# Optimization experiments

Measured on AMD Instinct MI355X. Metric: run time of the kernel, lower is better.

## Reference

```python
import jax, jax.numpy as jnp
import numpy as np

EPS = 1e-5

def layer_norm(x, g, b):
    m = jnp.mean(x, axis=-1, keepdims=True)
    v = jnp.var(x, axis=-1, keepdims=True)
    return (x - m) * jax.lax.rsqrt(v + EPS) * g + b

def setup_inputs() -> dict:
    key = jax.random.key(0)
    ks = jax.random.split(key, 10)
    A, T, c_s, c_z, c_atom, c_pair = 1024, 256, 384, 128, 128, 16
    tok = jax.random.randint(ks[0], (A,), 0, T)
    a2t = jax.nn.one_hot(tok, T, dtype=jnp.float32)  # [A, T] one-hot atom->token map
    return {
        "atom_to_token_index": a2t,
        "cl": jax.random.normal(ks[1], (A, c_atom), jnp.float32),
        "plm": jax.random.normal(ks[2], (A, A, c_pair), jnp.float32),
        "ql": jax.random.normal(ks[3], (A, c_atom), jnp.float32),
        "s_trunk": jax.random.normal(ks[4], (T, c_s), jnp.float32),
        "zij": jax.random.normal(ks[5], (T, T, c_z), jnp.float32),
        "rl": jax.random.normal(ks[6], (A, 3), jnp.float32),
        "ln_s_g": jnp.ones((c_s,), jnp.float32),
        "ln_s_b": jnp.zeros((c_s,), jnp.float32),
        "W_s": jax.random.normal(ks[7], (c_s, c_atom), jnp.float32) / np.sqrt(c_s),
        "ln_z_g": jnp.ones((c_z,), jnp.float32),
        "ln_z_b": jnp.zeros((c_z,), jnp.float32),
        "W_z": jax.random.normal(ks[8], (c_z, c_pair), jnp.float32) / np.sqrt(c_z),
        "W_r": jax.random.normal(ks[9], (3, c_atom), jnp.float32) / np.sqrt(3.0),
    }

def reference(atom_to_token_index, cl, plm, ql, s_trunk, zij, rl,
              ln_s_g, ln_s_b, W_s, ln_z_g, ln_z_b, W_z, W_r):
    a2t = atom_to_token_index  # [A, T]
    # token -> atom gather of single rep: sum_t a2t[a,t] * s_trunk[t,:]  -> [A, c_s]
    s_atom = jnp.einsum('at,tc->ac', a2t, s_trunk)
    cl = cl + layer_norm(s_atom, ln_s_g, ln_s_b) @ W_s  # [A, c_atom]
    # token-pair -> atom-pair gather: sum_{t,u} a2t[a,t] a2t[b,u] zij[t,u,:]
    # factored into two one-hot contractions (same math as the dense one-hot outer product)
    z_half = jnp.einsum('at,tuz->auz', a2t, zij)      # [A, T, c_z]
    z_atom = jnp.einsum('auz,bu->abz', z_half, a2t)    # [A, A, c_z]
    plm = plm + layer_norm(z_atom, ln_z_g, ln_z_b) @ W_z  # [A, A, c_pair]
    ql = ql + rl @ W_r  # [A, c_atom]
    return (cl, plm, ql)
```

## Files before the change

kernel.cpp:

```cpp
#include <hip/hip_runtime.h>

#define A_N 1024
#define T_N 256
#define CS 384
#define CZ 128
#define CA 128
#define CP 16
#define LN_EPS 1e-5f

typedef __bf16  bf16x8 __attribute__((ext_vector_type(8)));
typedef float   f32x4  __attribute__((ext_vector_type(4)));

#define WSTRIDE 136
#define ZSTRIDE 132

__global__ __launch_bounds__(256) void token_kernel(
        const float* __restrict__ s_trunk,
        const float* __restrict__ gs,
        const float* __restrict__ bs,
        const float* __restrict__ W_s,
        float* __restrict__ Ys,
        const float* __restrict__ zij,
        const float* __restrict__ gz,
        const float* __restrict__ bz,
        const float* __restrict__ W_z,
        float* __restrict__ Yz,
        const float* __restrict__ a2t,
        int* __restrict__ tok) {
    __shared__ float  zs[64 * ZSTRIDE];
    __shared__ __bf16 wb[CP * WSTRIDE];
    __shared__ float2 gb_part[16][16];
    __shared__ float  Gw_sh[CP], Bw_sh[CP];

    int tid = threadIdx.x;

    if (blockIdx.x < 256) {
        float*  xs    = zs;
        float2* sred2 = (float2*)(zs + 384);
        float*  part  = zs + 392;
        int t = blockIdx.x;
        float sum = 0.f, sq = 0.f;
        {
            float v = s_trunk[t * CS + tid];
            xs[tid] = v; sum = v; sq = v * v;
            if (tid < CS - 256) {
                float v2 = s_trunk[t * CS + 256 + tid];
                xs[256 + tid] = v2; sum += v2; sq += v2 * v2;
            }
        }
        #pragma unroll
        for (int off = 32; off > 0; off >>= 1) {
            sum += __shfl_down(sum, off);
            sq  += __shfl_down(sq,  off);
        }
        if ((tid & 63) == 0) sred2[tid >> 6] = make_float2(sum, sq);
        __syncthreads();
        float s_ = sred2[0].x + sred2[1].x + sred2[2].x + sred2[3].x;
        float ss = sred2[0].y + sred2[1].y + sred2[2].y + sred2[3].y;
        float m = s_ * (1.f / CS);
        float rstd = rsqrtf(ss * (1.f / CS) - m * m + LN_EPS);

        int col = tid & 127, seg = tid >> 7;
        float a0 = 0.f, a1 = 0.f, a2 = 0.f, a3 = 0.f;
        int k0 = seg * (CS / 2);
        for (int k = k0; k < k0 + CS / 2; k += 4) {
            float z0 = (xs[k + 0] - m) * rstd * gs[k + 0] + bs[k + 0];
            float z1 = (xs[k + 1] - m) * rstd * gs[k + 1] + bs[k + 1];
            float z2 = (xs[k + 2] - m) * rstd * gs[k + 2] + bs[k + 2];
            float z3 = (xs[k + 3] - m) * rstd * gs[k + 3] + bs[k + 3];
            a0 = fmaf(z0, W_s[(k + 0) * CA + col], a0);
            a1 = fmaf(z1, W_s[(k + 1) * CA + col], a1);
            a2 = fmaf(z2, W_s[(k + 2) * CA + col], a2);
            a3 = fmaf(z3, W_s[(k + 3) * CA + col], a3);
        }
        part[seg * 128 + col] = (a0 + a1) + (a2 + a3);
        __syncthreads();
        if (tid < 128) Ys[t * CA + tid] = part[tid] + part[128 + tid];
        return;
    }

    int b = blockIdx.x - 256;

    { float v = a2t[(size_t)b * T_N + tid]; if (v > 0.5f) tok[b] = tid; }

    {
        int j = tid & 15, seg = tid >> 4;
        float sg = 0.f, sb = 0.f;
        #pragma unroll
        for (int i = 0; i < 8; ++i) {
            int k = seg * 8 + i;
            float w = W_z[k * CP + j];
            float gw = gz[k] * w;
            wb[j * WSTRIDE + k] = (__bf16)gw;
            sg += gw;
            sb = fmaf(bz[k], w, sb);
        }
        gb_part[seg][j] = make_float2(sg, sb);
    }

    size_t R0 = (size_t)b * 64;
    const float4* zg = (const float4*)(zij + R0 * CZ);
    #pragma unroll
    for (int it = 0; it < 8; ++it) {
        int g = it * 256 + tid;
        int row = g >> 5, c4 = g & 31;
        *(float4*)&zs[row * ZSTRIDE + c4 * 4] = zg[g];
    }
    __syncthreads();

    if (tid < CP) {
        float sg = 0.f, sb = 0.f;
        #pragma unroll
        for (int s = 0; s < 16; ++s) { float2 p = gb_part[s][tid]; sg += p.x; sb += p.y; }
        Gw_sh[tid] = sg; Bw_sh[tid] = sb;
    }

    int wave = tid >> 6, lane = tid & 63;
    int m16  = lane & 15, quad = lane >> 4;
    int r_loc = wave * 16 + m16;

    float4 xv[8];
    #pragma unroll
    for (int s = 0; s < 4; ++s) {
        xv[2 * s]     = *(const float4*)&zs[r_loc * ZSTRIDE + quad * 8 + 32 * s];
        xv[2 * s + 1] = *(const float4*)&zs[r_loc * ZSTRIDE + quad * 8 + 32 * s + 4];
    }

    float zsum = 0.f, zsq = 0.f;
    #pragma unroll
    for (int i = 0; i < 8; ++i) {
        float4 v = xv[i];
        zsum += (v.x + v.y) + (v.z + v.w);
        zsq  += v.x * v.x + v.y * v.y + v.z * v.z + v.w * v.w;
    }
    zsum += __shfl_xor(zsum, 16);  zsq += __shfl_xor(zsq, 16);
    zsum += __shfl_xor(zsum, 32);  zsq += __shfl_xor(zsq, 32);
    float mval = zsum * (1.f / CZ);
    float rstd = rsqrtf(zsq * (1.f / CZ) - mval * mval + LN_EPS);

    __syncthreads();

    f32x4 acc = {0.f, 0.f, 0.f, 0.f};
    #pragma unroll
    for (int s = 0; s < 4; ++s) {
        float4 v0 = xv[2 * s], v1 = xv[2 * s + 1];
        bf16x8 af;
        af[0] = (__bf16)v0.x; af[1] = (__bf16)v0.y;
        af[2] = (__bf16)v0.z; af[3] = (__bf16)v0.w;
        af[4] = (__bf16)v1.x; af[5] = (__bf16)v1.y;
        af[6] = (__bf16)v1.z; af[7] = (__bf16)v1.w;
        bf16x8 bfv = *(const bf16x8*)&wb[m16 * WSTRIDE + quad * 8 + 32 * s];
        acc = __builtin_amdgcn_mfma_f32_16x16x32_bf16(af, bfv, acc, 0, 0, 0);
    }

    float gwj = Gw_sh[m16], bwj = Bw_sh[m16];
    size_t obase = R0 + wave * 16;
    #pragma unroll
    for (int i = 0; i < 4; ++i) {
        int r = quad * 4 + i;
        float mi = __shfl(mval, r);
        float ri = __shfl(rstd, r);
        float y = ri * (acc[i] - mi * gwj) + bwj;
        Yz[(obase + r) * CP + m16] = y;
    }
}

__global__ __launch_bounds__(512) void atom_plm_kernel(
        const float* __restrict__ plm,
        const float* __restrict__ Yz,
        const int* __restrict__ tok,
        const float* __restrict__ cl,
        const float* __restrict__ ql,
        const float* __restrict__ rl,
        const float* __restrict__ Ys,
        const float* __restrict__ W_r,
        float* __restrict__ out_cl,
        float* __restrict__ out_plm,
        float* __restrict__ out_ql) {
    __shared__ int    tok_sh[A_N];
    __shared__ float4 yz_sh[T_N * CP / 4];

    int a = blockIdx.x;
    int tid = threadIdx.x;
    int ta = tok[a];

    if (tid < 256) ((int4*)tok_sh)[tid] = ((const int4*)tok)[tid];

    const float4* yrow = (const float4*)(Yz + (size_t)ta * (T_N * CP));
    #pragma unroll
    for (int p = 0; p < 2; ++p) {
        int j = p * 512 + tid;
        yz_sh[j ^ ((j >> 3) & 7)] = yrow[j];
    }

    const float4* prow = (const float4*)(plm + (size_t)a * (A_N * CP));
    float4 pf[4];
    #pragma unroll
    for (int i = 0; i < 4; ++i) pf[i] = prow[i * 512 + tid];

    if (tid < 128) {
        out_cl[(size_t)a * CA + tid] = cl[(size_t)a * CA + tid]
                                     + Ys[(size_t)ta * CA + tid];
    } else if (tid < 256) {
        int c = tid - 128;
        float r0 = rl[a * 3 + 0], r1 = rl[a * 3 + 1], r2 = rl[a * 3 + 2];
        out_ql[(size_t)a * CA + c] = ql[(size_t)a * CA + c]
            + fmaf(r0, W_r[c], fmaf(r1, W_r[CA + c], r2 * W_r[2 * CA + c]));
    }
    __syncthreads();

    float4* orow = (float4*)(out_plm + (size_t)a * (A_N * CP));

    float4 sh2[4];
    #pragma unroll
    for (int i = 0; i < 4; ++i) sh2[i] = prow[(i + 4) * 512 + tid];

    #pragma unroll
    for (int i = 0; i < 4; ++i) {
        int f4 = i * 512 + tid;
        int tb = tok_sh[f4 >> 2];
        int x  = tb * 4 + (f4 & 3);
        float4 yv = yz_sh[x ^ ((x >> 3) & 7)];
        float4 o;
        o.x = pf[i].x + yv.x; o.y = pf[i].y + yv.y;
        o.z = pf[i].z + yv.z; o.w = pf[i].w + yv.w;
        orow[f4] = o;
    }
    #pragma unroll
    for (int i = 0; i < 4; ++i) {
        int f4 = (i + 4) * 512 + tid;
        int tb = tok_sh[f4 >> 2];
        int x  = tb * 4 + (f4 & 3);
        float4 yv = yz_sh[x ^ ((x >> 3) & 7)];
        float4 o;
        o.x = sh2[i].x + yv.x; o.y = sh2[i].y + yv.y;
        o.z = sh2[i].z + yv.z; o.w = sh2[i].w + yv.w;
        orow[f4] = o;
    }
}

extern "C" void kernel_launch(void* const* d_in, const int* in_sizes, int n_in,
                              void* d_out, int out_size, void* d_ws, size_t ws_size,
                              hipStream_t stream) {
    const float* a2t     = (const float*)d_in[0];
    const float* cl      = (const float*)d_in[1];
    const float* plm     = (const float*)d_in[2];
    const float* ql      = (const float*)d_in[3];
    const float* s_trunk = (const float*)d_in[4];
    const float* zij     = (const float*)d_in[5];
    const float* rl      = (const float*)d_in[6];
    const float* ln_s_g  = (const float*)d_in[7];
    const float* ln_s_b  = (const float*)d_in[8];
    const float* W_s     = (const float*)d_in[9];
    const float* ln_z_g  = (const float*)d_in[10];
    const float* ln_z_b  = (const float*)d_in[11];
    const float* W_z     = (const float*)d_in[12];
    const float* W_r     = (const float*)d_in[13];

    int*   tok = (int*)d_ws;
    float* Ys  = (float*)((char*)d_ws + 4096);
    float* Yz  = (float*)((char*)d_ws + 4096 + 131072);

    float* out_cl  = (float*)d_out;
    float* out_plm = out_cl + A_N * CA;
    float* out_ql  = out_plm + (size_t)A_N * A_N * CP;

    token_kernel<<<256 + T_N * T_N / 64, 256, 0, stream>>>(
        s_trunk, ln_s_g, ln_s_b, W_s, Ys,
        zij, ln_z_g, ln_z_b, W_z, Yz,
        a2t, tok);
    atom_plm_kernel<<<A_N, 512, 0, stream>>>(
        plm, Yz, tok, cl, ql, rl, Ys, W_r,
        out_cl, out_plm, out_ql);
}
```

Measured before the change: 180.2 us.

## Split each atom row across two 256-thread blocks with all plm loads issued upfront

The atom_plm kernel now launches two 256-thread blocks per atom row, each handling half of the 1024x16 plm row. Each block issues all eight float4 loads before any compute, and empty asm barriers pin those values in registers so the loads are not interleaved with the stores. The aim is more blocks in flight and more memory requests outstanding per wave on a bandwidth-bound kernel. In exchange, each block now loads the 16 KB Yz token row and the 4 KB tok table itself, doubling that shared-memory staging traffic and LDS use per row.

```diff
diff --git a/kernel.cpp b/kernel.cpp
--- a/kernel.cpp
+++ b/kernel.cpp
@@ -165,7 +165,7 @@
     }
 }
 
-__global__ __launch_bounds__(512) void atom_plm_kernel(
+__global__ __launch_bounds__(256, 6) void atom_plm_kernel(
         const float* __restrict__ plm,
         const float* __restrict__ Yz,
         const int* __restrict__ tok,
@@ -180,61 +180,53 @@
     __shared__ int    tok_sh[A_N];
     __shared__ float4 yz_sh[T_N * CP / 4];
 
-    int a = blockIdx.x;
-    int tid = threadIdx.x;
-    int ta = tok[a];
-
-    if (tid < 256) ((int4*)tok_sh)[tid] = ((const int4*)tok)[tid];
+    int bid  = blockIdx.x;
+    int a    = bid >> 1;
+    int half = bid & 1;
+    int tid  = threadIdx.x;
+    int ta   = tok[a];
+
+    ((int4*)tok_sh)[tid] = ((const int4*)tok)[tid];
 
     const float4* yrow = (const float4*)(Yz + (size_t)ta * (T_N * CP));
     #pragma unroll
-    for (int p = 0; p < 2; ++p) {
-        int j = p * 512 + tid;
+    for (int p = 0; p < 4; ++p) {
+        int j = p * 256 + tid;
         yz_sh[j ^ ((j >> 3) & 7)] = yrow[j];
     }
 
-    const float4* prow = (const float4*)(plm + (size_t)a * (A_N * CP));
-    float4 pf[4];
-    #pragma unroll
-    for (int i = 0; i < 4; ++i) pf[i] = prow[i * 512 + tid];
-
-    if (tid < 128) {
-        out_cl[(size_t)a * CA + tid] = cl[(size_t)a * CA + tid]
-                                     + Ys[(size_t)ta * CA + tid];
-    } else if (tid < 256) {
-        int c = tid - 128;
-        float r0 = rl[a * 3 + 0], r1 = rl[a * 3 + 1], r2 = rl[a * 3 + 2];
-        out_ql[(size_t)a * CA + c] = ql[(size_t)a * CA + c]
-            + fmaf(r0, W_r[c], fmaf(r1, W_r[CA + c], r2 * W_r[2 * CA + c]));
+    if (half == 0) {
+        if (tid < 128) {
+            out_cl[(size_t)a * CA + tid] = cl[(size_t)a * CA + tid]
+                                         + Ys[(size_t)ta * CA + tid];
+        } else {
+            int c = tid - 128;
+            float r0 = rl[a * 3 + 0], r1 = rl[a * 3 + 1], r2 = rl[a * 3 + 2];
+            out_ql[(size_t)a * CA + c] = ql[(size_t)a * CA + c]
+                + fmaf(r0, W_r[c], fmaf(r1, W_r[CA + c], r2 * W_r[2 * CA + c]));
+        }
     }
     __syncthreads();
 
-    float4* orow = (float4*)(out_plm + (size_t)a * (A_N * CP));
-
-    float4 sh2[4];
-    #pragma unroll
-    for (int i = 0; i < 4; ++i) sh2[i] = prow[(i + 4) * 512 + tid];
-
-    #pragma unroll
-    for (int i = 0; i < 4; ++i) {
-        int f4 = i * 512 + tid;
+    const float4* prow = (const float4*)(plm     + (size_t)a * (A_N * CP));
+    float4*       orow = (float4*)      (out_plm + (size_t)a * (A_N * CP));
+    int base = half * 2048 + tid;
+
+    float4 pf[8];
+    #pragma unroll
+    for (int i = 0; i < 8; ++i) pf[i] = prow[base + i * 256];
+
+    #pragma unroll
+    for (int i = 0; i < 8; ++i) {
+        asm volatile("" : "+v"(pf[i].x), "+v"(pf[i].y),
+                          "+v"(pf[i].z), "+v"(pf[i].w));
+        int f4 = base + i * 256;
         int tb = tok_sh[f4 >> 2];
         int x  = tb * 4 + (f4 & 3);
         float4 yv = yz_sh[x ^ ((x >> 3) & 7)];
         float4 o;
         o.x = pf[i].x + yv.x; o.y = pf[i].y + yv.y;
         o.z = pf[i].z + yv.z; o.w = pf[i].w + yv.w;
-        orow[f4] = o;
-    }
-    #pragma unroll
-    for (int i = 0; i < 4; ++i) {
-        int f4 = (i + 4) * 512 + tid;
-        int tb = tok_sh[f4 >> 2];
-        int x  = tb * 4 + (f4 & 3);
-        float4 yv = yz_sh[x ^ ((x >> 3) & 7)];
-        float4 o;
-        o.x = sh2[i].x + yv.x; o.y = sh2[i].y + yv.y;
-        o.z = sh2[i].z + yv.z; o.w = sh2[i].w + yv.w;
         orow[f4] = o;
     }
 }
@@ -269,7 +261,7 @@
         s_trunk, ln_s_g, ln_s_b, W_s, Ys,
         zij, ln_z_g, ln_z_b, W_z, Yz,
         a2t, tok);
-    atom_plm_kernel<<<A_N, 512, 0, stream>>>(
+    atom_plm_kernel<<<2 * A_N, 256, 0, stream>>>(
         plm, Yz, tok, cl, ql, rl, Ys, W_r,
         out_cl, out_plm, out_ql);
 }
```

After: 179.6 us. Within noise of the previous version (-0.3%).
